# Kernel tuning notes

Hardware: AMD Instinct MI355X
Metric: run time of the kernel (lower is better)

The kernel has to match this reference:

```python
import jax, jax.numpy as jnp
from jax import lax
import numpy as np

HIDDEN = 256
UID_EMB, LOC_EMB, WD_EMB, HR_EMB = 64, 128, 16, 16
UID_NUM, LOC_NUM = 5000, 50000
S, L, C = 32, 32, 128   # steps, current-trace prefix length, candidates per step
HN, LH = 32, 64         # history traces, history trace length
EMB = UID_EMB + LOC_EMB + WD_EMB + HR_EMB  # 224


def setup_inputs() -> dict:
    key = jax.random.key(0)
    ks = jax.random.split(key, 20)
    def lin(k, o, i, s=0.05):
        return jax.random.normal(k, (o, i), jnp.float32) * s
    return {
        "uid": 7,
        "current_trace": jnp.stack([
            jax.random.randint(ks[0], (S, L), 0, LOC_NUM),
            jax.random.randint(ks[1], (S, L), 0, 7),
            jax.random.randint(ks[2], (S, L), 0, 24)], axis=-1),
        "history_trace": jnp.stack([
            jax.random.randint(ks[3], (HN, LH), 0, LOC_NUM),
            jax.random.randint(ks[4], (HN, LH), 0, 7),
            jax.random.randint(ks[5], (HN, LH), 0, 24)], axis=-1),
        "candidate_set": jax.random.randint(ks[6], (S, C), 0, LOC_NUM),
        "uid_emb": jax.random.normal(ks[7], (UID_NUM, UID_EMB), jnp.float32),
        "loc_emb": jax.random.normal(ks[8], (LOC_NUM, LOC_EMB), jnp.float32),
        "weekday_emb": jax.random.normal(ks[9], (7, WD_EMB), jnp.float32),
        "hour_emb": jax.random.normal(ks[10], (24, HR_EMB), jnp.float32),
        "W_ih": lin(ks[11], 3 * HIDDEN, EMB),
        "W_hh": lin(ks[12], 3 * HIDDEN, HIDDEN),
        "b_ih": jnp.zeros((3 * HIDDEN,), jnp.float32),
        "b_hh": jnp.zeros((3 * HIDDEN,), jnp.float32),
        "intra_w1": lin(ks[13], HIDDEN, HIDDEN),
        "intra_w2": lin(ks[14], HIDDEN, HIDDEN),
        "intra_out": lin(ks[15], 1, HIDDEN),
        "inter_w1": lin(ks[16], HIDDEN, HIDDEN),
        "inter_w2": lin(ks[17], HIDDEN, HIDDEN),
        "inter_out": lin(ks[18], 1, HIDDEN),
        "score_w": lin(ks[19], 1, HIDDEN),
    }


def _gru(x, W_ih, W_hh, b_ih, b_hh):
    # x: [B, T, D] -> all hidden states [B, T, H]; single-layer torch GRU equations
    B = x.shape[0]
    H = W_hh.shape[1]
    x_proj = x @ W_ih.T + b_ih  # [B, T, 3H], precomputed input projection
    def step(h, xp):
        gh = h @ W_hh.T + b_hh
        xr, xz, xn = jnp.split(xp, 3, axis=-1)
        hr, hz, hn = jnp.split(gh, 3, axis=-1)
        r = jax.nn.sigmoid(xr + hr)
        z = jax.nn.sigmoid(xz + hz)
        n = jnp.tanh(xn + r * hn)
        h_new = (1.0 - z) * n + z * h
        return h_new, h_new
    h0 = jnp.zeros((B, H), x.dtype)
    _, hs = lax.scan(step, h0, jnp.swapaxes(x_proj, 0, 1))
    return jnp.swapaxes(hs, 0, 1)


def _forward(uid, current_trace, history_trace, candidate_set,
             uid_emb, loc_emb, weekday_emb, hour_emb,
             W_ih, W_hh, b_ih, b_hh,
             intra_w1, intra_w2, intra_out,
             inter_w1, inter_w2, inter_out, score_w):
    def encode(trace):  # [B, T, 3] int -> [B, H]
        B, T, _ = trace.shape
        u = jnp.broadcast_to(uid_emb[uid][None, None, :], (B, T, UID_EMB))
        e = jnp.concatenate([u,
                             loc_emb[trace[:, :, 0]],
                             weekday_emb[trace[:, :, 1]],
                             hour_emb[trace[:, :, 2]]], axis=-1)
        hs = _gru(e, W_ih, W_hh, b_ih, b_hh)
        # intra-trajectory attention: query = last hidden state, key = all hidden states
        qh = jax.nn.relu(hs[:, -1, :] @ intra_w1.T)[:, None, :]
        kh = jax.nn.relu(hs @ intra_w2.T)
        a = (jnp.tanh(qh + kh) @ intra_out.T)[..., 0]  # [B, T]
        w = jax.nn.softmax(a, axis=1)
        return jnp.einsum('bt,bth->bh', w, hs)

    hist_hidden = encode(history_trace)  # [HN, H]

    S_, L_, _ = current_trace.shape
    C_ = candidate_set.shape[1]
    last_time = current_trace[:, -1, 1:3]  # [S, 2] weekday/hour of last observed point
    cand_point = jnp.concatenate(
        [candidate_set[..., None],
         jnp.broadcast_to(last_time[:, None, :], (S_, C_, 2))], axis=-1)  # [S, C, 3]
    cand_trace = jnp.concatenate(
        [jnp.broadcast_to(current_trace[:, None], (S_, C_, L_, 3)),
         cand_point[:, :, None, :]], axis=2)  # [S, C, L+1, 3]
    cand_hidden = encode(cand_trace.reshape(S_ * C_, L_ + 1, 3))  # [S*C, H]

    # inter-trajectory attention; history key is shared across all candidates
    qh = jax.nn.relu(cand_hidden @ inter_w1.T)      # [S*C, H]
    kh = jax.nn.relu(hist_hidden @ inter_w2.T)      # [HN, H]
    a = (jnp.tanh(qh[:, None, :] + kh[None]) @ inter_out.T)[..., 0]  # [S*C, HN]
    w = jax.nn.softmax(a, axis=1)
    moving = w @ hist_hidden                        # [S*C, H]

    scores = (moving @ score_w.T)[:, 0].reshape(S_, C_)
    probs = jax.nn.softmax(scores, axis=1)          # softmax over candidate set per step
    return probs, moving.reshape(S_, C_, HIDDEN)


def reference(uid, current_trace, history_trace, candidate_set,
              uid_emb, loc_emb, weekday_emb, hour_emb,
              W_ih, W_hh, b_ih, b_hh,
              intra_w1, intra_w2, intra_out,
              inter_w1, inter_w2, inter_out, score_w):
    return _forward(uid, current_trace, history_trace, candidate_set,
                    uid_emb, loc_emb, weekday_emb, hour_emb,
                    W_ih, W_hh, b_ih, b_hh,
                    intra_w1, intra_w2, intra_out,
                    inter_w1, inter_w2, inter_out, score_w)
```

## Files before the change

### kernel.cpp

```cpp
#include <hip/hip_runtime.h>
#include <math.h>

#define NHID   256
#define NEMB   224

constexpr int OFF_BASE = 0;
constexpr int OFF_WDP  = 768;
constexpr int OFF_HRP  = OFF_WDP + 7*768;
constexpr int OFF_XPH  = OFF_HRP + 24*768;
constexpr int OFF_XPC  = OFF_XPH + 32*64*768;
constexpr int OFF_HSH  = OFF_XPC + 32*32*768;
constexpr int OFF_HSC  = OFF_HSH + 32*64*256;
constexpr int OFF_GHL  = OFF_HSC + 32*32*256;
constexpr int OFF_QHH  = OFF_GHL + 32*768;
constexpr int OFF_HC   = OFF_QHH + 32*256;
constexpr int OFF_KHH  = OFF_HC  + 4096*256;
constexpr int OFF_KHSH = OFF_KHH + 32*64*256;
constexpr int OFF_KHC  = OFF_KHSH+ 32*32*256;
constexpr int OFF_QHC  = OFF_KHC + 4096*256;
constexpr int OFF_HIST = OFF_QHC + 4096*256;
constexpr int OFF_CHID = OFF_HIST+ 32*256;
constexpr int OFF_QH2  = OFF_CHID+ 4096*256;
constexpr int OFF_KH2  = OFF_QH2 + 4096*256;
constexpr int OFF_SC   = OFF_KH2 + 32*256;
constexpr int OFF_W16  = OFF_KHH;

__device__ __forceinline__ float sigm(float x) { return 1.0f / (1.0f + __expf(-x)); }

typedef _Float16 half2_t __attribute__((ext_vector_type(2)));

__device__ __forceinline__ float fdot2f(unsigned int a, unsigned int b, float c) {
#if __has_builtin(__builtin_amdgcn_fdot2)
  return __builtin_amdgcn_fdot2(__builtin_bit_cast(half2_t, a),
                                __builtin_bit_cast(half2_t, b), c, false);
#else
  half2_t x = __builtin_bit_cast(half2_t, a);
  half2_t y = __builtin_bit_cast(half2_t, b);
  return c + (float)x[0] * (float)y[0] + (float)x[1] * (float)y[1];
#endif
}

__device__ __forceinline__ unsigned int packh(float a, float b) {
  unsigned short lo = __builtin_bit_cast(unsigned short, (_Float16)a);
  unsigned short hi = __builtin_bit_cast(unsigned short, (_Float16)b);
  return (unsigned int)lo | ((unsigned int)hi << 16);
}

__global__ __launch_bounds__(256) void k_prep(const int* uid, const float* uid_emb,
                                              const float* wde, const float* hre,
                                              const float* W_ih, const float* b_ih,
                                              float* ws) {
  __shared__ __align__(16) float ev[64];
  int blk = blockIdx.x, tid = threadIdx.x;
  if (blk == 0) {
    if (tid < 64) ev[tid] = uid_emb[uid[0] * 64 + tid];
    __syncthreads();
    #pragma unroll
    for (int jj = 0; jj < 3; ++jj) {
      int j = tid + jj * 256;
      float acc = b_ih[j];
      const float* wr = W_ih + j * NEMB;
      #pragma unroll
      for (int k = 0; k < 64; k += 4) {
        float4 w = *(const float4*)(wr + k);
        acc += ev[k]*w.x + ev[k+1]*w.y + ev[k+2]*w.z + ev[k+3]*w.w;
      }
      ws[OFF_BASE + j] = acc;
    }
  } else if (blk < 8) {
    int wd = blk - 1;
    if (tid < 16) ev[tid] = wde[wd * 16 + tid];
    __syncthreads();
    #pragma unroll
    for (int jj = 0; jj < 3; ++jj) {
      int j = tid + jj * 256;
      float acc = 0.f;
      const float* wr = W_ih + j * NEMB + 192;
      #pragma unroll
      for (int k = 0; k < 16; k += 4) {
        float4 w = *(const float4*)(wr + k);
        acc += ev[k]*w.x + ev[k+1]*w.y + ev[k+2]*w.z + ev[k+3]*w.w;
      }
      ws[OFF_WDP + wd * 768 + j] = acc;
    }
  } else {
    int hr = blk - 8;
    if (tid < 16) ev[tid] = hre[hr * 16 + tid];
    __syncthreads();
    #pragma unroll
    for (int jj = 0; jj < 3; ++jj) {
      int j = tid + jj * 256;
      float acc = 0.f;
      const float* wr = W_ih + j * NEMB + 208;
      #pragma unroll
      for (int k = 0; k < 16; k += 4) {
        float4 w = *(const float4*)(wr + k);
        acc += ev[k]*w.x + ev[k+1]*w.y + ev[k+2]*w.z + ev[k+3]*w.w;
      }
      ws[OFF_HRP + hr * 768 + j] = acc;
    }
  }
}

__global__ __launch_bounds__(256) void k_pack(const float* W_hh, float* ws) {
  int idx = blockIdx.x * 256 + threadIdx.x;
  int i4 = idx & 31, j = idx >> 5;
  const float4* p = (const float4*)(W_hh + j * 256 + i4 * 8);
  float4 a = p[0], b = p[1];
  uint4 o;
  o.x = packh(a.x, a.y); o.y = packh(a.z, a.w);
  o.z = packh(b.x, b.y); o.w = packh(b.z, b.w);
  ((uint4*)((unsigned int*)ws + OFF_W16))[i4 * 768 + j] = o;
}

__global__ __launch_bounds__(256) void k_xproj(const int* cur_tr, const int* hist_tr,
                                               const float* loc_emb, const float* W_ih,
                                               float* ws) {
  __shared__ float Ws[768][17];
  __shared__ float Xs[16][20];
  __shared__ int s_wd[16], s_hr[16], s_loc[16];
  int blk = blockIdx.x, tid = threadIdx.x;
  int r0 = blk * 16;

  if (tid < 16) {
    int row = r0 + tid;
    const int* tr; int idx;
    if (row < 2048) { tr = hist_tr; idx = row; } else { tr = cur_tr; idx = row - 2048; }
    s_loc[tid] = tr[idx * 3];
    s_wd[tid]  = tr[idx * 3 + 1];
    s_hr[tid]  = tr[idx * 3 + 2];
  }
  __syncthreads();

  float accA[16], accB[16], accC[16];
  #pragma unroll
  for (int r = 0; r < 16; ++r) { accA[r] = 0.f; accB[r] = 0.f; accC[r] = 0.f; }

  for (int kb = 0; kb < 8; ++kb) {
    for (int i = tid; i < 768 * 4; i += 256) {
      int j = i >> 2, q = (i & 3) * 4;
      float4 w = *(const float4*)&W_ih[j * NEMB + 64 + kb * 16 + q];
      Ws[j][q] = w.x; Ws[j][q+1] = w.y; Ws[j][q+2] = w.z; Ws[j][q+3] = w.w;
    }
    if (tid < 64) {
      int r = tid >> 2, q = (tid & 3) * 4;
      float4 x = *(const float4*)&loc_emb[s_loc[r] * 128 + kb * 16 + q];
      Xs[q][r] = x.x; Xs[q+1][r] = x.y; Xs[q+2][r] = x.z; Xs[q+3][r] = x.w;
    }
    __syncthreads();
    #pragma unroll
    for (int kk = 0; kk < 16; ++kk) {
      float wa = Ws[tid][kk], wb = Ws[tid + 256][kk], wc = Ws[tid + 512][kk];
      float4 x0 = *(const float4*)&Xs[kk][0];
      float4 x1 = *(const float4*)&Xs[kk][4];
      float4 x2 = *(const float4*)&Xs[kk][8];
      float4 x3 = *(const float4*)&Xs[kk][12];
      float xv[16] = {x0.x,x0.y,x0.z,x0.w, x1.x,x1.y,x1.z,x1.w,
                      x2.x,x2.y,x2.z,x2.w, x3.x,x3.y,x3.z,x3.w};
      #pragma unroll
      for (int r = 0; r < 16; ++r) {
        accA[r] += xv[r] * wa; accB[r] += xv[r] * wb; accC[r] += xv[r] * wc;
      }
    }
    __syncthreads();
  }

  float bA = ws[OFF_BASE + tid], bB = ws[OFF_BASE + 256 + tid], bC = ws[OFF_BASE + 512 + tid];
  for (int r = 0; r < 16; ++r) {
    int row = r0 + r;
    float* outp = (row < 2048) ? (ws + OFF_XPH + row * 768)
                               : (ws + OFF_XPC + (row - 2048) * 768);
    const float* wdp = ws + OFF_WDP + s_wd[r] * 768;
    const float* hrp = ws + OFF_HRP + s_hr[r] * 768;
    outp[tid]       = accA[r] + bA + wdp[tid]       + hrp[tid];
    outp[256 + tid] = accB[r] + bB + wdp[256 + tid] + hrp[256 + tid];
    outp[512 + tid] = accC[r] + bC + wdp[512 + tid] + hrp[512 + tid];
  }
}

__global__ __launch_bounds__(768) void k_gru(const float* b_hh, const float* intra_w1,
                                             float* ws) {
  __shared__ __align__(16) float gh[768];
  __shared__ __align__(16) float h32[256];
  __shared__ __align__(16) unsigned short h16[256];
  int w = blockIdx.x, tid = threadIdx.x;
  int T; const float* xp; float* hs;
  if (w < 32) { T = 64; xp = ws + OFF_XPH + w * 64 * 768; hs = ws + OFF_HSH + w * 64 * 256; }
  else        { T = 32; int b = w - 32; xp = ws + OFF_XPC + b * 32 * 768; hs = ws + OFF_HSC + b * 32 * 256; }

  uint4 wreg[32];
  {
    const uint4* wp = (const uint4*)((const unsigned int*)ws + OFF_W16) + tid;
    #pragma unroll
    for (int i = 0; i < 32; ++i) wreg[i] = wp[i * 768];
  }
  float bh = b_hh[tid];
  if (tid < 256) { h32[tid] = 0.f; h16[tid] = 0; }
  __syncthreads();

  for (int t = 0; t < T; ++t) {
    float xr, xz, xn;
    if (tid < 256) {
      xr = xp[t * 768 + tid];
      xz = xp[t * 768 + 256 + tid];
      xn = xp[t * 768 + 512 + tid];
    }
    float acc = bh;
    const uint4* hp = (const uint4*)h16;
    #pragma unroll
    for (int i = 0; i < 32; ++i) {
      uint4 hv = hp[i];
      acc = fdot2f(wreg[i].x, hv.x, acc);
      acc = fdot2f(wreg[i].y, hv.y, acc);
      acc = fdot2f(wreg[i].z, hv.z, acc);
      acc = fdot2f(wreg[i].w, hv.w, acc);
    }
    gh[tid] = acc;
    __syncthreads();
    if (tid < 256) {
      float r  = sigm(xr + gh[tid]);
      float z  = sigm(xz + gh[256 + tid]);
      float n  = tanhf(xn + r * gh[512 + tid]);
      float hn = (1.f - z) * n + z * h32[tid];
      h32[tid] = hn;
      hs[t * 256 + tid] = hn;
      h16[tid] = __builtin_bit_cast(unsigned short, (_Float16)hn);
    }
    __syncthreads();
  }

  if (w < 32) {
    if (tid < 256) {
      float acc = 0.f;
      const float* r1 = intra_w1 + tid * 256;
      #pragma unroll 16
      for (int k = 0; k < 256; k += 4) {
        float4 wv = *(const float4*)(r1 + k);
        float4 hv = *(const float4*)&h32[k];
        acc += hv.x*wv.x + hv.y*wv.y + hv.z*wv.z + hv.w*wv.w;
      }
      ws[OFF_QHH + w * 256 + tid] = fmaxf(acc, 0.f);
    }
  } else {
    float acc = bh;
    const uint4* hp = (const uint4*)h16;
    #pragma unroll
    for (int i = 0; i < 32; ++i) {
      uint4 hv = hp[i];
      acc = fdot2f(wreg[i].x, hv.x, acc);
      acc = fdot2f(wreg[i].y, hv.y, acc);
      acc = fdot2f(wreg[i].z, hv.z, acc);
      acc = fdot2f(wreg[i].w, hv.w, acc);
    }
    ws[OFF_GHL + (w - 32) * 768 + tid] = acc;
  }
}

__global__ __launch_bounds__(256) void k_cand(const int* cur_tr, const int* cand_set,
                                              const float* loc_emb, const float* W_ih,
                                              float* ws) {
  __shared__ float Ws[768][17];
  __shared__ float Xs[16][20];
  int blk = blockIdx.x, tid = threadIdx.x;
  int r0 = blk * 16;
  int s = r0 >> 7;

  float accA[16], accB[16], accC[16];
  #pragma unroll
  for (int r = 0; r < 16; ++r) { accA[r] = 0.f; accB[r] = 0.f; accC[r] = 0.f; }

  for (int kb = 0; kb < 8; ++kb) {
    for (int i = tid; i < 768 * 4; i += 256) {
      int j = i >> 2, q = (i & 3) * 4;
      float4 w = *(const float4*)&W_ih[j * NEMB + 64 + kb * 16 + q];
      Ws[j][q] = w.x; Ws[j][q+1] = w.y; Ws[j][q+2] = w.z; Ws[j][q+3] = w.w;
    }
    if (tid < 64) {
      int r = tid >> 2, q = (tid & 3) * 4;
      float4 x = *(const float4*)&loc_emb[cand_set[r0 + r] * 128 + kb * 16 + q];
      Xs[q][r] = x.x; Xs[q+1][r] = x.y; Xs[q+2][r] = x.z; Xs[q+3][r] = x.w;
    }
    __syncthreads();
    #pragma unroll
    for (int kk = 0; kk < 16; ++kk) {
      float wa = Ws[tid][kk], wb = Ws[tid + 256][kk], wc = Ws[tid + 512][kk];
      float4 x0 = *(const float4*)&Xs[kk][0];
      float4 x1 = *(const float4*)&Xs[kk][4];
      float4 x2 = *(const float4*)&Xs[kk][8];
      float4 x3 = *(const float4*)&Xs[kk][12];
      float xv[16] = {x0.x,x0.y,x0.z,x0.w, x1.x,x1.y,x1.z,x1.w,
                      x2.x,x2.y,x2.z,x2.w, x3.x,x3.y,x3.z,x3.w};
      #pragma unroll
      for (int r = 0; r < 16; ++r) {
        accA[r] += xv[r] * wa; accB[r] += xv[r] * wb; accC[r] += xv[r] * wc;
      }
    }
    __syncthreads();
  }

  int last = s * 32 + 31;
  int wd = cur_tr[last * 3 + 1], hr = cur_tr[last * 3 + 2];
  const float* wdp = ws + OFF_WDP + wd * 768;
  const float* hrp = ws + OFF_HRP + hr * 768;
  float xbA = ws[OFF_BASE + tid]       + wdp[tid]       + hrp[tid];
  float xbB = ws[OFF_BASE + 256 + tid] + wdp[256 + tid] + hrp[256 + tid];
  float xbC = ws[OFF_BASE + 512 + tid] + wdp[512 + tid] + hrp[512 + tid];
  float ghr = ws[OFF_GHL + s * 768 + tid];
  float ghz = ws[OFF_GHL + s * 768 + 256 + tid];
  float ghn = ws[OFF_GHL + s * 768 + 512 + tid];
  float hp  = ws[OFF_HSC + last * 256 + tid];

  for (int r = 0; r < 16; ++r) {
    float rr = sigm(xbA + accA[r] + ghr);
    float zz = sigm(xbB + accB[r] + ghz);
    float nn = tanhf(xbC + accC[r] + ghn);
    float hn = (1.f - zz) * nn + zz * hp;
    ws[OFF_HC + (r0 + r) * 256 + tid] = hn;
  }
}

__device__ __forceinline__ void proj_body(const float* in, float* out, const float* W,
                                          int r0, int tid) {
  __shared__ float Ws[256][33];
  __shared__ float Xs[32][36];
  int c0 = tid & 63, rg = (tid >> 6) * 8;
  float acc[4][8];
  #pragma unroll
  for (int c = 0; c < 4; ++c)
    #pragma unroll
    for (int r = 0; r < 8; ++r) acc[c][r] = 0.f;

  for (int kb = 0; kb < 8; ++kb) {
    for (int i = tid; i < 256 * 8; i += 256) {
      int j = i >> 3, q = (i & 7) * 4;
      float4 v = *(const float4*)&W[j * 256 + kb * 32 + q];
      Ws[j][q] = v.x; Ws[j][q+1] = v.y; Ws[j][q+2] = v.z; Ws[j][q+3] = v.w;
    }
    {
      int r = tid >> 3, q = (tid & 7) * 4;
      float4 v = *(const float4*)&in[(r0 + r) * 256 + kb * 32 + q];
      Xs[q][r] = v.x; Xs[q+1][r] = v.y; Xs[q+2][r] = v.z; Xs[q+3][r] = v.w;
    }
    __syncthreads();
    #pragma unroll
    for (int kk = 0; kk < 32; ++kk) {
      float w0 = Ws[c0][kk], w1 = Ws[c0 + 64][kk], w2 = Ws[c0 + 128][kk], w3 = Ws[c0 + 192][kk];
      float4 xa = *(const float4*)&Xs[kk][rg];
      float4 xb = *(const float4*)&Xs[kk][rg + 4];
      float xv[8] = {xa.x,xa.y,xa.z,xa.w, xb.x,xb.y,xb.z,xb.w};
      #pragma unroll
      for (int r = 0; r < 8; ++r) {
        acc[0][r] += xv[r] * w0; acc[1][r] += xv[r] * w1;
        acc[2][r] += xv[r] * w2; acc[3][r] += xv[r] * w3;
      }
    }
    __syncthreads();
  }
  #pragma unroll
  for (int c = 0; c < 4; ++c)
    for (int r = 0; r < 8; ++r)
      out[(r0 + rg + r) * 256 + c0 + c * 64] = fmaxf(acc[c][r], 0.f);
}

__global__ __launch_bounds__(256) void k_proj_intra(const float* intra_w1, const float* intra_w2,
                                                    float* ws) {
  int blk = blockIdx.x, tid = threadIdx.x;
  const float* in; float* out; const float* W; int r0;
  if (blk < 64)       { in = ws + OFF_HSH; out = ws + OFF_KHH;  W = intra_w2; r0 = blk * 32; }
  else if (blk < 96)  { in = ws + OFF_HSC; out = ws + OFF_KHSH; W = intra_w2; r0 = (blk - 64) * 32; }
  else if (blk < 224) { in = ws + OFF_HC;  out = ws + OFF_KHC;  W = intra_w2; r0 = (blk - 96) * 32; }
  else                { in = ws + OFF_HC;  out = ws + OFF_QHC;  W = intra_w1; r0 = (blk - 224) * 32; }
  proj_body(in, out, W, r0, tid);
}

__global__ __launch_bounds__(256) void k_proj_inter(const float* inter_w1, const float* inter_w2,
                                                    float* ws) {
  int blk = blockIdx.x, tid = threadIdx.x;
  const float* in; float* out; const float* W; int r0;
  if (blk < 128) { in = ws + OFF_CHID; out = ws + OFF_QH2; W = inter_w1; r0 = blk * 32; }
  else           { in = ws + OFF_HIST; out = ws + OFF_KH2; W = inter_w2; r0 = 0; }
  proj_body(in, out, W, r0, tid);
}

__global__ __launch_bounds__(256) void k_hist_attn(const float* intra_out, float* ws) {
  __shared__ __align__(16) float a[64];
  int b = blockIdx.x, tid = threadIdx.x;
  int wv = tid >> 6, lane = tid & 63;
  const float* qh = ws + OFF_QHH + b * 256;
  const float* kh = ws + OFF_KHH + b * 64 * 256;
  const float* hs = ws + OFF_HSH + b * 64 * 256;

  float4 q4  = *(const float4*)&qh[lane * 4];
  float4 io4 = *(const float4*)&intra_out[lane * 4];
  for (int t = wv; t < 64; t += 4) {
    float4 k4 = *(const float4*)&kh[t * 256 + lane * 4];
    float p = tanhf(q4.x + k4.x) * io4.x + tanhf(q4.y + k4.y) * io4.y +
              tanhf(q4.z + k4.z) * io4.z + tanhf(q4.w + k4.w) * io4.w;
    #pragma unroll
    for (int off = 32; off; off >>= 1) p += __shfl_down(p, off);
    if (lane == 0) a[t] = p;
  }
  __syncthreads();
  if (tid < 64) {
    float v = a[tid];
    float m = v;
    #pragma unroll
    for (int off = 32; off; off >>= 1) m = fmaxf(m, __shfl_xor(m, off));
    float e = __expf(v - m);
    float ssum = e;
    #pragma unroll
    for (int off = 32; off; off >>= 1) ssum += __shfl_xor(ssum, off);
    a[tid] = e / ssum;
  }
  __syncthreads();
  float acc = 0.f;
  for (int t = 0; t < 64; ++t) acc += a[t] * hs[t * 256 + tid];
  ws[OFF_HIST + b * 256 + tid] = acc;
}

__global__ __launch_bounds__(64) void k_cand_attn(const float* intra_out, float* ws) {
  int bId = blockIdx.x;
  int s = bId >> 7;
  int lane = threadIdx.x;
  const float* qh  = ws + OFF_QHC  + bId * 256;
  const float* khs = ws + OFF_KHSH + s * 32 * 256;
  const float* khc = ws + OFF_KHC  + bId * 256;
  const float* hsc = ws + OFF_HSC  + s * 32 * 256;
  const float* hc  = ws + OFF_HC   + bId * 256;

  float4 q4  = *(const float4*)&qh[lane * 4];
  float4 io4 = *(const float4*)&intra_out[lane * 4];
  float aa[33];
  float m = -1e30f;
  for (int t = 0; t < 33; ++t) {
    const float* kk = (t < 32) ? &khs[t * 256] : khc;
    float4 k4 = *(const float4*)&kk[lane * 4];
    float p = tanhf(q4.x + k4.x) * io4.x + tanhf(q4.y + k4.y) * io4.y +
              tanhf(q4.z + k4.z) * io4.z + tanhf(q4.w + k4.w) * io4.w;
    #pragma unroll
    for (int off = 32; off; off >>= 1) p += __shfl_xor(p, off);
    aa[t] = p;
    m = fmaxf(m, p);
  }
  float ssum = 0.f;
  #pragma unroll
  for (int t = 0; t < 33; ++t) { aa[t] = __expf(aa[t] - m); ssum += aa[t]; }
  float inv = 1.f / ssum;
  float ax = 0.f, ay = 0.f, az = 0.f, aw = 0.f;
  for (int t = 0; t < 32; ++t) {
    float wt = aa[t] * inv;
    float4 hv = *(const float4*)&hsc[t * 256 + lane * 4];
    ax += wt * hv.x; ay += wt * hv.y; az += wt * hv.z; aw += wt * hv.w;
  }
  {
    float wt = aa[32] * inv;
    float4 hv = *(const float4*)&hc[lane * 4];
    ax += wt * hv.x; ay += wt * hv.y; az += wt * hv.z; aw += wt * hv.w;
  }
  float4 o; o.x = ax; o.y = ay; o.z = az; o.w = aw;
  *(float4*)&ws[OFF_CHID + bId * 256 + lane * 4] = o;
}

__global__ __launch_bounds__(64) void k_inter_attn(const float* inter_out, const float* score_w,
                                                   float* ws, float* d_out) {
  int bId = blockIdx.x;
  int lane = threadIdx.x;
  const float* qh   = ws + OFF_QH2 + bId * 256;
  const float* kh2  = ws + OFF_KH2;
  const float* hist = ws + OFF_HIST;

  float4 q4  = *(const float4*)&qh[lane * 4];
  float4 io4 = *(const float4*)&inter_out[lane * 4];
  float aa[32];
  float m = -1e30f;
  for (int t = 0; t < 32; ++t) {
    float4 k4 = *(const float4*)&kh2[t * 256 + lane * 4];
    float p = tanhf(q4.x + k4.x) * io4.x + tanhf(q4.y + k4.y) * io4.y +
              tanhf(q4.z + k4.z) * io4.z + tanhf(q4.w + k4.w) * io4.w;
    #pragma unroll
    for (int off = 32; off; off >>= 1) p += __shfl_xor(p, off);
    aa[t] = p;
    m = fmaxf(m, p);
  }
  float ssum = 0.f;
  #pragma unroll
  for (int t = 0; t < 32; ++t) { aa[t] = __expf(aa[t] - m); ssum += aa[t]; }
  float inv = 1.f / ssum;
  float ax = 0.f, ay = 0.f, az = 0.f, aw = 0.f;
  for (int t = 0; t < 32; ++t) {
    float wt = aa[t] * inv;
    float4 hv = *(const float4*)&hist[t * 256 + lane * 4];
    ax += wt * hv.x; ay += wt * hv.y; az += wt * hv.z; aw += wt * hv.w;
  }
  float4 o; o.x = ax; o.y = ay; o.z = az; o.w = aw;
  *(float4*)&d_out[4096 + bId * 256 + lane * 4] = o;
  float4 sw = *(const float4*)&score_w[lane * 4];
  float sc = ax*sw.x + ay*sw.y + az*sw.z + aw*sw.w;
  #pragma unroll
  for (int off = 32; off; off >>= 1) sc += __shfl_xor(sc, off);
  if (lane == 0) ws[OFF_SC + bId] = sc;
}

__global__ __launch_bounds__(64) void k_probs(const float* ws, float* d_out) {
  int s = blockIdx.x, lane = threadIdx.x;
  float v0 = ws[OFF_SC + s * 128 + lane];
  float v1 = ws[OFF_SC + s * 128 + 64 + lane];
  float m = fmaxf(v0, v1);
  #pragma unroll
  for (int off = 32; off; off >>= 1) m = fmaxf(m, __shfl_xor(m, off));
  float e0 = __expf(v0 - m), e1 = __expf(v1 - m);
  float ssum = e0 + e1;
  #pragma unroll
  for (int off = 32; off; off >>= 1) ssum += __shfl_xor(ssum, off);
  float inv = 1.f / ssum;
  d_out[s * 128 + lane] = e0 * inv;
  d_out[s * 128 + 64 + lane] = e1 * inv;
}

extern "C" void kernel_launch(void* const* d_in, const int* in_sizes, int n_in,
                              void* d_out, int out_size, void* d_ws, size_t ws_size,
                              hipStream_t stream) {
  const int*   uid      = (const int*)  d_in[0];
  const int*   cur_tr   = (const int*)  d_in[1];
  const int*   hist_tr  = (const int*)  d_in[2];
  const int*   cand_set = (const int*)  d_in[3];
  const float* uid_emb  = (const float*)d_in[4];
  const float* loc_emb  = (const float*)d_in[5];
  const float* wde      = (const float*)d_in[6];
  const float* hre      = (const float*)d_in[7];
  const float* W_ih     = (const float*)d_in[8];
  const float* W_hh     = (const float*)d_in[9];
  const float* b_ih     = (const float*)d_in[10];
  const float* b_hh     = (const float*)d_in[11];
  const float* intra_w1 = (const float*)d_in[12];
  const float* intra_w2 = (const float*)d_in[13];
  const float* intra_out= (const float*)d_in[14];
  const float* inter_w1 = (const float*)d_in[15];
  const float* inter_w2 = (const float*)d_in[16];
  const float* inter_out= (const float*)d_in[17];
  const float* score_w  = (const float*)d_in[18];
  float* ws  = (float*)d_ws;
  float* out = (float*)d_out;

  hipLaunchKernelGGL(k_prep,       dim3(32),   dim3(256), 0, stream, uid, uid_emb, wde, hre, W_ih, b_ih, ws);
  hipLaunchKernelGGL(k_pack,       dim3(96),   dim3(256), 0, stream, W_hh, ws);
  hipLaunchKernelGGL(k_xproj,      dim3(192),  dim3(256), 0, stream, cur_tr, hist_tr, loc_emb, W_ih, ws);
  hipLaunchKernelGGL(k_gru,        dim3(64),   dim3(768), 0, stream, b_hh, intra_w1, ws);
  hipLaunchKernelGGL(k_cand,       dim3(256),  dim3(256), 0, stream, cur_tr, cand_set, loc_emb, W_ih, ws);
  hipLaunchKernelGGL(k_proj_intra, dim3(352),  dim3(256), 0, stream, intra_w1, intra_w2, ws);
  hipLaunchKernelGGL(k_hist_attn,  dim3(32),   dim3(256), 0, stream, intra_out, ws);
  hipLaunchKernelGGL(k_cand_attn,  dim3(4096), dim3(64),  0, stream, intra_out, ws);
  hipLaunchKernelGGL(k_proj_inter, dim3(129),  dim3(256), 0, stream, inter_w1, inter_w2, ws);
  hipLaunchKernelGGL(k_inter_attn, dim3(4096), dim3(64),  0, stream, inter_out, score_w, ws, out);
  hipLaunchKernelGGL(k_probs,      dim3(32),   dim3(64),  0, stream, ws, out);
}
```

Before: 454.9 us.

## Restructure GRU recurrence to 256 threads with double-buffered hidden state

The GRU kernel now runs 256 threads per block, each computing all three gate rows in registers. A double-buffered fp16 hidden vector cuts each timestep to a single barrier and drops the shared gate staging buffer. The W_hh packing kernel is folded into the prep kernel to save a launch, and tanhf is replaced with an exp-based fast tanh in the GRU and attention kernels. The three-gate register footprint (96 uint4 per thread) could cause spills, and the fast tanh slightly changes numerics.

```diff
diff --git a/kernel.cpp b/kernel.cpp
--- a/kernel.cpp
+++ b/kernel.cpp
@@ -26,6 +26,9 @@
 constexpr int OFF_W16  = OFF_KHH;
 
 __device__ __forceinline__ float sigm(float x) { return 1.0f / (1.0f + __expf(-x)); }
+__device__ __forceinline__ float tanhf_fast(float x) {
+  return 1.f - 2.f / (__expf(2.f * x) + 1.f);
+}
 
 typedef _Float16 half2_t __attribute__((ext_vector_type(2)));
 
@@ -46,12 +49,27 @@
   return (unsigned int)lo | ((unsigned int)hi << 16);
 }
 
+#define DOT4(acc, wv, hv) \
+  acc = fdot2f((wv).x, (hv).x, acc); acc = fdot2f((wv).y, (hv).y, acc); \
+  acc = fdot2f((wv).z, (hv).z, acc); acc = fdot2f((wv).w, (hv).w, acc);
+
 __global__ __launch_bounds__(256) void k_prep(const int* uid, const float* uid_emb,
                                               const float* wde, const float* hre,
                                               const float* W_ih, const float* b_ih,
-                                              float* ws) {
+                                              const float* W_hh, float* ws) {
   __shared__ __align__(16) float ev[64];
   int blk = blockIdx.x, tid = threadIdx.x;
+  if (blk >= 32) {
+    int idx = (blk - 32) * 256 + tid;
+    int i4 = idx & 31, j = idx >> 5;
+    const float4* p = (const float4*)(W_hh + j * 256 + i4 * 8);
+    float4 a = p[0], b = p[1];
+    uint4 o;
+    o.x = packh(a.x, a.y); o.y = packh(a.z, a.w);
+    o.z = packh(b.x, b.y); o.w = packh(b.z, b.w);
+    ((uint4*)((unsigned int*)ws + OFF_W16))[i4 * 768 + j] = o;
+    return;
+  }
   if (blk == 0) {
     if (tid < 64) ev[tid] = uid_emb[uid[0] * 64 + tid];
     __syncthreads();
@@ -100,17 +118,6 @@
       ws[OFF_HRP + hr * 768 + j] = acc;
     }
   }
-}
-
-__global__ __launch_bounds__(256) void k_pack(const float* W_hh, float* ws) {
-  int idx = blockIdx.x * 256 + threadIdx.x;
-  int i4 = idx & 31, j = idx >> 5;
-  const float4* p = (const float4*)(W_hh + j * 256 + i4 * 8);
-  float4 a = p[0], b = p[1];
-  uint4 o;
-  o.x = packh(a.x, a.y); o.y = packh(a.z, a.w);
-  o.z = packh(b.x, b.y); o.w = packh(b.z, b.w);
-  ((uint4*)((unsigned int*)ws + OFF_W16))[i4 * 768 + j] = o;
 }
 
 __global__ __launch_bounds__(256) void k_xproj(const int* cur_tr, const int* hist_tr,
@@ -178,81 +185,81 @@
   }
 }
 
-__global__ __launch_bounds__(768) void k_gru(const float* b_hh, const float* intra_w1,
-                                             float* ws) {
-  __shared__ __align__(16) float gh[768];
-  __shared__ __align__(16) float h32[256];
-  __shared__ __align__(16) unsigned short h16[256];
+__global__ __launch_bounds__(256, 1) void k_gru(const float* b_hh, const float* intra_w1,
+                                                float* ws) {
+  __shared__ __align__(16) unsigned short h16[2][256];
+  __shared__ __align__(16) float hfin[256];
   int w = blockIdx.x, tid = threadIdx.x;
   int T; const float* xp; float* hs;
   if (w < 32) { T = 64; xp = ws + OFF_XPH + w * 64 * 768; hs = ws + OFF_HSH + w * 64 * 256; }
   else        { T = 32; int b = w - 32; xp = ws + OFF_XPC + b * 32 * 768; hs = ws + OFF_HSC + b * 32 * 256; }
 
-  uint4 wreg[32];
+  uint4 wra[32], wrb[32], wrc[32];
   {
-    const uint4* wp = (const uint4*)((const unsigned int*)ws + OFF_W16) + tid;
-    #pragma unroll
-    for (int i = 0; i < 32; ++i) wreg[i] = wp[i * 768];
-  }
-  float bh = b_hh[tid];
-  if (tid < 256) { h32[tid] = 0.f; h16[tid] = 0; }
+    const uint4* wp = (const uint4*)((const unsigned int*)ws + OFF_W16);
+    #pragma unroll
+    for (int i = 0; i < 32; ++i) {
+      wra[i] = wp[i * 768 + tid];
+      wrb[i] = wp[i * 768 + tid + 256];
+      wrc[i] = wp[i * 768 + tid + 512];
+    }
+  }
+  float bha = b_hh[tid], bhb = b_hh[tid + 256], bhc = b_hh[tid + 512];
+  h16[0][tid] = 0;
+  float hprev = 0.f;
   __syncthreads();
 
+  int cur = 0;
   for (int t = 0; t < T; ++t) {
-    float xr, xz, xn;
-    if (tid < 256) {
-      xr = xp[t * 768 + tid];
-      xz = xp[t * 768 + 256 + tid];
-      xn = xp[t * 768 + 512 + tid];
-    }
-    float acc = bh;
-    const uint4* hp = (const uint4*)h16;
-    #pragma unroll
-    for (int i = 0; i < 32; ++i) {
-      uint4 hv = hp[i];
-      acc = fdot2f(wreg[i].x, hv.x, acc);
-      acc = fdot2f(wreg[i].y, hv.y, acc);
-      acc = fdot2f(wreg[i].z, hv.z, acc);
-      acc = fdot2f(wreg[i].w, hv.w, acc);
-    }
-    gh[tid] = acc;
-    __syncthreads();
-    if (tid < 256) {
-      float r  = sigm(xr + gh[tid]);
-      float z  = sigm(xz + gh[256 + tid]);
-      float n  = tanhf(xn + r * gh[512 + tid]);
-      float hn = (1.f - z) * n + z * h32[tid];
-      h32[tid] = hn;
-      hs[t * 256 + tid] = hn;
-      h16[tid] = __builtin_bit_cast(unsigned short, (_Float16)hn);
-    }
-    __syncthreads();
+    float xr = xp[t * 768 + tid];
+    float xz = xp[t * 768 + 256 + tid];
+    float xn = xp[t * 768 + 512 + tid];
+    const uint4* hp = (const uint4*)h16[cur];
+    float a0 = bha, a1 = 0.f, b0 = bhb, b1 = 0.f, c0 = bhc, c1 = 0.f;
+    #pragma unroll
+    for (int i = 0; i < 32; i += 2) {
+      uint4 h0 = hp[i];
+      DOT4(a0, wra[i], h0) DOT4(b0, wrb[i], h0) DOT4(c0, wrc[i], h0)
+      uint4 h1 = hp[i + 1];
+      DOT4(a1, wra[i+1], h1) DOT4(b1, wrb[i+1], h1) DOT4(c1, wrc[i+1], h1)
+    }
+    float r  = sigm(xr + a0 + a1);
+    float z  = sigm(xz + b0 + b1);
+    float n  = tanhf_fast(xn + r * (c0 + c1));
+    float hn = (1.f - z) * n + z * hprev;
+    hprev = hn;
+    hs[t * 256 + tid] = hn;
+    h16[cur ^ 1][tid] = (unsigned short)__builtin_bit_cast(unsigned short, (_Float16)hn);
+    __syncthreads();
+    cur ^= 1;
   }
 
   if (w < 32) {
-    if (tid < 256) {
-      float acc = 0.f;
-      const float* r1 = intra_w1 + tid * 256;
-      #pragma unroll 16
-      for (int k = 0; k < 256; k += 4) {
-        float4 wv = *(const float4*)(r1 + k);
-        float4 hv = *(const float4*)&h32[k];
-        acc += hv.x*wv.x + hv.y*wv.y + hv.z*wv.z + hv.w*wv.w;
-      }
-      ws[OFF_QHH + w * 256 + tid] = fmaxf(acc, 0.f);
-    }
+    hfin[tid] = hprev;
+    __syncthreads();
+    float acc = 0.f;
+    const float* r1 = intra_w1 + tid * 256;
+    #pragma unroll 16
+    for (int k = 0; k < 256; k += 4) {
+      float4 wv = *(const float4*)(r1 + k);
+      float4 hv = *(const float4*)&hfin[k];
+      acc += hv.x*wv.x + hv.y*wv.y + hv.z*wv.z + hv.w*wv.w;
+    }
+    ws[OFF_QHH + w * 256 + tid] = fmaxf(acc, 0.f);
   } else {
-    float acc = bh;
-    const uint4* hp = (const uint4*)h16;
-    #pragma unroll
-    for (int i = 0; i < 32; ++i) {
-      uint4 hv = hp[i];
-      acc = fdot2f(wreg[i].x, hv.x, acc);
-      acc = fdot2f(wreg[i].y, hv.y, acc);
-      acc = fdot2f(wreg[i].z, hv.z, acc);
-      acc = fdot2f(wreg[i].w, hv.w, acc);
-    }
-    ws[OFF_GHL + (w - 32) * 768 + tid] = acc;
+    const uint4* hp = (const uint4*)h16[cur];
+    float a0 = bha, a1 = 0.f, b0 = bhb, b1 = 0.f, c0 = bhc, c1 = 0.f;
+    #pragma unroll
+    for (int i = 0; i < 32; i += 2) {
+      uint4 h0 = hp[i];
+      DOT4(a0, wra[i], h0) DOT4(b0, wrb[i], h0) DOT4(c0, wrc[i], h0)
+      uint4 h1 = hp[i + 1];
+      DOT4(a1, wra[i+1], h1) DOT4(b1, wrb[i+1], h1) DOT4(c1, wrc[i+1], h1)
+    }
+    int b = w - 32;
+    ws[OFF_GHL + b * 768 + tid]       = a0 + a1;
+    ws[OFF_GHL + b * 768 + 256 + tid] = b0 + b1;
+    ws[OFF_GHL + b * 768 + 512 + tid] = c0 + c1;
   }
 }
 
@@ -313,7 +320,7 @@
   for (int r = 0; r < 16; ++r) {
     float rr = sigm(xbA + accA[r] + ghr);
     float zz = sigm(xbB + accB[r] + ghz);
-    float nn = tanhf(xbC + accC[r] + ghn);
+    float nn = tanhf_fast(xbC + accC[r] + ghn);
     float hn = (1.f - zz) * nn + zz * hp;
     ws[OFF_HC + (r0 + r) * 256 + tid] = hn;
   }
@@ -394,8 +401,8 @@
   float4 io4 = *(const float4*)&intra_out[lane * 4];
   for (int t = wv; t < 64; t += 4) {
     float4 k4 = *(const float4*)&kh[t * 256 + lane * 4];
-    float p = tanhf(q4.x + k4.x) * io4.x + tanhf(q4.y + k4.y) * io4.y +
-              tanhf(q4.z + k4.z) * io4.z + tanhf(q4.w + k4.w) * io4.w;
+    float p = tanhf_fast(q4.x + k4.x) * io4.x + tanhf_fast(q4.y + k4.y) * io4.y +
+              tanhf_fast(q4.z + k4.z) * io4.z + tanhf_fast(q4.w + k4.w) * io4.w;
     #pragma unroll
     for (int off = 32; off; off >>= 1) p += __shfl_down(p, off);
     if (lane == 0) a[t] = p;
@@ -435,8 +442,8 @@
   for (int t = 0; t < 33; ++t) {
     const float* kk = (t < 32) ? &khs[t * 256] : khc;
     float4 k4 = *(const float4*)&kk[lane * 4];
-    float p = tanhf(q4.x + k4.x) * io4.x + tanhf(q4.y + k4.y) * io4.y +
-              tanhf(q4.z + k4.z) * io4.z + tanhf(q4.w + k4.w) * io4.w;
+    float p = tanhf_fast(q4.x + k4.x) * io4.x + tanhf_fast(q4.y + k4.y) * io4.y +
+              tanhf_fast(q4.z + k4.z) * io4.z + tanhf_fast(q4.w + k4.w) * io4.w;
     #pragma unroll
     for (int off = 32; off; off >>= 1) p += __shfl_xor(p, off);
     aa[t] = p;
@@ -475,8 +482,8 @@
   float m = -1e30f;
   for (int t = 0; t < 32; ++t) {
     float4 k4 = *(const float4*)&kh2[t * 256 + lane * 4];
-    float p = tanhf(q4.x + k4.x) * io4.x + tanhf(q4.y + k4.y) * io4.y +
-              tanhf(q4.z + k4.z) * io4.z + tanhf(q4.w + k4.w) * io4.w;
+    float p = tanhf_fast(q4.x + k4.x) * io4.x + tanhf_fast(q4.y + k4.y) * io4.y +
+              tanhf_fast(q4.z + k4.z) * io4.z + tanhf_fast(q4.w + k4.w) * io4.w;
     #pragma unroll
     for (int off = 32; off; off >>= 1) p += __shfl_xor(p, off);
     aa[t] = p;
@@ -542,10 +549,9 @@
   float* ws  = (float*)d_ws;
   float* out = (float*)d_out;
 
-  hipLaunchKernelGGL(k_prep,       dim3(32),   dim3(256), 0, stream, uid, uid_emb, wde, hre, W_ih, b_ih, ws);
-  hipLaunchKernelGGL(k_pack,       dim3(96),   dim3(256), 0, stream, W_hh, ws);
+  hipLaunchKernelGGL(k_prep,       dim3(128),  dim3(256), 0, stream, uid, uid_emb, wde, hre, W_ih, b_ih, W_hh, ws);
   hipLaunchKernelGGL(k_xproj,      dim3(192),  dim3(256), 0, stream, cur_tr, hist_tr, loc_emb, W_ih, ws);
-  hipLaunchKernelGGL(k_gru,        dim3(64),   dim3(768), 0, stream, b_hh, intra_w1, ws);
+  hipLaunchKernelGGL(k_gru,        dim3(64),   dim3(256), 0, stream, b_hh, intra_w1, ws);
   hipLaunchKernelGGL(k_cand,       dim3(256),  dim3(256), 0, stream, cur_tr, cand_set, loc_emb, W_ih, ws);
   hipLaunchKernelGGL(k_proj_intra, dim3(352),  dim3(256), 0, stream, intra_w1, intra_w2, ws);
   hipLaunchKernelGGL(k_hist_attn,  dim3(32),   dim3(256), 0, stream, intra_out, ws);
```

After: 536.5 us. 1.18x slower.
